# Kernel tuning notes

Hardware: AMD Instinct MI355X
Metric: run time of the kernel (lower is better)

The kernel has to match this reference:

```python
import jax, jax.numpy as jnp
import numpy as np
from jax import lax

B = 16
IMG = 384
P = 16
C = 3
DIM = 256
DEPTH = 6
HEADS = 4
DH = 64
INNER = HEADS * DH  # 256
MLP = 512
NC = 21
HP = IMG // P       # 24
N = HP * HP         # 576
PD = C * P * P      # 768
K = 16
SCALE = DH ** -0.5
NEG = -1e9


def _ln(x, g, b):
    mu = x.mean(-1, keepdims=True)
    var = ((x - mu) ** 2).mean(-1, keepdims=True)
    return (x - mu) / jnp.sqrt(var + 1e-5) * g + b


def _conv(x, w, b):
    y = lax.conv_general_dilated(x, w, (1, 1), 'SAME',
                                 dimension_numbers=('NCHW', 'OIHW', 'NCHW'))
    return y + b[None, :, None, None]


def _up2(x):
    b, c, h, w = x.shape
    return jax.image.resize(x, (b, c, 2 * h, 2 * w), 'bilinear')


def _attn(x, g, bt, qkv_w, out_w, out_b, alpha):
    xn = _ln(x, g, bt)
    qkv = xn @ qkv_w                              # [B,N,3*INNER]
    q, k, v = jnp.split(qkv, 3, axis=-1)
    def heads(t):
        return t.reshape(B, N, HEADS, DH).transpose(0, 2, 1, 3)  # b h n d
    q, k, v = heads(q), heads(k), heads(v)
    dots = jnp.einsum('bhid,bhjd->bhij', q, k) * SCALE           # [B,H,N,N]
    vals, idx = lax.top_k(dots, K)                               # [B,H,N,K]
    bi = jnp.arange(B)[:, None, None, None]
    hi = jnp.arange(HEADS)[None, :, None, None]
    ni = jnp.arange(N)[None, None, :, None]
    sparse = jnp.full(dots.shape, NEG, dots.dtype).at[bi, hi, ni, idx].set(vals)
    sparse_attn = jax.nn.softmax(sparse, axis=-1)
    global_attn = jax.nn.softmax(dots, axis=-1)
    a = jnp.clip(alpha, 0.0, 1.0)
    attn = (1 - a) * sparse_attn + a * global_attn
    out = jnp.einsum('bhij,bhjd->bhid', attn, v)                 # [B,H,N,DH]
    out = out.transpose(0, 2, 1, 3).reshape(B, N, INNER)
    return out @ out_w + out_b


def _forward(img, patch_w, patch_b, pos_emb,
             ln1_g, ln1_b, qkv_w, out_w, out_b, alpha,
             ln2_g, ln2_b, ff_w1, ff_b1, ff_w2, ff_b2,
             lnf_g, lnf_b,
             conv1_w, conv1_b, conv2_w, conv2_b, conv3_w, conv3_b):
    # patchify: b c (h p1) (w p2) -> b (h w) (p1 p2 c)
    x = img.reshape(B, C, HP, P, HP, P).transpose(0, 2, 4, 3, 5, 1).reshape(B, N, PD)
    x = x @ patch_w + patch_b + pos_emb
    for i in range(DEPTH):
        x = x + _attn(x, ln1_g[i], ln1_b[i], qkv_w[i], out_w[i], out_b[i], alpha[i])
        h = _ln(x, ln2_g[i], ln2_b[i])
        h = jax.nn.gelu(h @ ff_w1[i] + ff_b1[i], approximate=False)
        x = x + h @ ff_w2[i] + ff_b2[i]
    x = _ln(x, lnf_g, lnf_b)
    x = x.transpose(0, 2, 1).reshape(B, DIM, HP, HP)             # b d h w
    x = jax.nn.relu(_conv(x, conv1_w, conv1_b))
    x = _up2(x)
    x = jax.nn.relu(_conv(x, conv2_w, conv2_b))
    x = _up2(x)
    x = _conv(x, conv3_w, conv3_b)
    return jax.image.resize(x, (B, NC, IMG, IMG), 'bilinear')


def setup_inputs() -> dict:
    key = jax.random.key(0)
    ks = jax.random.split(key, 16)
    s = 0.02
    d = {
        'img': jax.random.normal(ks[0], (B, C, IMG, IMG), jnp.float32),
        'patch_w': jax.random.normal(ks[1], (PD, DIM)) * s,
        'patch_b': jnp.zeros((DIM,)),
        'pos_emb': jax.random.normal(ks[2], (1, N, DIM)) * s,
        'ln1_g': jnp.ones((DEPTH, DIM)), 'ln1_b': jnp.zeros((DEPTH, DIM)),
        'qkv_w': jax.random.normal(ks[3], (DEPTH, DIM, 3 * INNER)) * s,
        'out_w': jax.random.normal(ks[4], (DEPTH, INNER, DIM)) * s,
        'out_b': jnp.zeros((DEPTH, DIM)),
        'alpha': jnp.full((DEPTH,), 0.2),
        'ln2_g': jnp.ones((DEPTH, DIM)), 'ln2_b': jnp.zeros((DEPTH, DIM)),
        'ff_w1': jax.random.normal(ks[5], (DEPTH, DIM, MLP)) * s,
        'ff_b1': jnp.zeros((DEPTH, MLP)),
        'ff_w2': jax.random.normal(ks[6], (DEPTH, MLP, DIM)) * s,
        'ff_b2': jnp.zeros((DEPTH, DIM)),
        'lnf_g': jnp.ones((DIM,)), 'lnf_b': jnp.zeros((DIM,)),
        'conv1_w': jax.random.normal(ks[7], (DIM // 2, DIM, 3, 3)) * s,
        'conv1_b': jnp.zeros((DIM // 2,)),
        'conv2_w': jax.random.normal(ks[8], (DIM // 4, DIM // 2, 3, 3)) * s,
        'conv2_b': jnp.zeros((DIM // 4,)),
        'conv3_w': jax.random.normal(ks[9], (NC, DIM // 4, 1, 1)) * s,
        'conv3_b': jnp.zeros((NC,)),
    }
    return d


def reference(img, patch_w, patch_b, pos_emb,
              ln1_g, ln1_b, qkv_w, out_w, out_b, alpha,
              ln2_g, ln2_b, ff_w1, ff_b1, ff_w2, ff_b2,
              lnf_g, lnf_b,
              conv1_w, conv1_b, conv2_w, conv2_b, conv3_w, conv3_b):
    return _forward(img, patch_w, patch_b, pos_emb,
                    ln1_g, ln1_b, qkv_w, out_w, out_b, alpha,
                    ln2_g, ln2_b, ff_w1, ff_b1, ff_w2, ff_b2,
                    lnf_g, lnf_b,
                    conv1_w, conv1_b, conv2_w, conv2_b, conv3_w, conv3_b)
```

## Files before the change

kernel.cpp:

```cpp
#include <hip/hip_runtime.h>
#include <cfloat>
#include <cmath>

constexpr int NB    = 16;
constexpr int IMGSZ = 384;
constexpr int PSZ   = 16;
constexpr int NCH   = 3;
constexpr int DMODEL= 256;
constexpr int DEPTH = 6;
constexpr int NHEAD = 4;
constexpr int DHEAD = 64;
constexpr int DQKV  = 768;
constexpr int DMLP  = 512;
constexpr int NCLS  = 21;
constexpr int HPATCH= 24;
constexpr int NTOK  = 576;
constexpr int NPD   = 768;
constexpr int TOPK  = 16;
constexpr int NROWS = NB * NTOK;
constexpr int OUT_TOTAL = NB * NCLS * IMGSZ * IMGSZ;

constexpr int RPB    = 16;
constexpr int NBLK   = NTOK / RPB;
constexpr int CHUNK  = 64;
constexpr int NCHUNK = NTOK / CHUNK;
constexpr int SCP    = 577;

typedef __attribute__((ext_vector_type(8))) short bf16x8;
typedef __attribute__((ext_vector_type(4))) float f32x4;

__device__ __forceinline__ unsigned short f2bf(float f) {
    unsigned u = __builtin_bit_cast(unsigned, f);
    unsigned r = (u + 0x7FFFu + ((u >> 16) & 1u)) >> 16;
    return (unsigned short)r;
}
__device__ __forceinline__ float bf2f(unsigned short h) {
    unsigned u = ((unsigned)h) << 16;
    return __builtin_bit_cast(float, u);
}

__global__ __launch_bounds__(256) void k_castT(const float* __restrict__ src,
                                               unsigned short* __restrict__ dst,
                                               int K, int N) {
    int t = blockIdx.x * 256 + threadIdx.x;
    if (t >= K * N) return;
    size_t base = (size_t)blockIdx.y * K * N;
    int n = t / K, k = t - n * K;
    dst[base + t] = f2bf(src[base + (size_t)k * N + n]);
}

template <int IC>
__global__ __launch_bounds__(256) void k_castConv(const float* __restrict__ src,
                                                  unsigned short* __restrict__ dst,
                                                  int OC) {
    int t = blockIdx.x * 256 + threadIdx.x;
    if (t >= OC * 9 * IC) return;
    int oc = t / (9 * IC);
    int r = t - oc * 9 * IC;
    int tap = r / IC, ic = r - tap * IC;
    dst[t] = f2bf(src[((size_t)(oc * IC + ic)) * 9 + tap]);
}

__global__ __launch_bounds__(256) void k_patchify(const float* __restrict__ img,
                                                  unsigned short* __restrict__ A) {
    int t = blockIdx.x * 256 + threadIdx.x;
    if (t >= NROWS * NPD) return;
    int r  = t / NPD, pd = t - r * NPD;
    int b  = r / NTOK, n = r - b * NTOK;
    int hy = n / HPATCH, hx = n - hy * HPATCH;
    int c  = pd % NCH;  int q = pd / NCH;
    int p2 = q % PSZ;   int p1 = q / PSZ;
    A[t] = f2bf(img[(((size_t)(b * NCH + c)) * IMGSZ + hy * PSZ + p1) * IMGSZ + hx * PSZ + p2]);
}

template <int BM, int BN, int EPI, int CIN>
__global__ __launch_bounds__(256) void k_mm(
    const unsigned short* __restrict__ Abf,
    const unsigned short* __restrict__ Wt,
    const float* __restrict__ bias,
    const float* __restrict__ extra,
    float* __restrict__ outf,
    unsigned short* __restrict__ outb,
    unsigned short* __restrict__ outb2,
    int M, int Nn, int K, int H, int Wd, int gxd, int gyd)
{
    constexpr int MF = BM / 32;
    constexpr int NF = BN / 32;
    constexpr bool GATHER = (CIN > 0);
    constexpr int AREP = BM * 4 / 256;
    constexpr int BREP = BN * 4 / 256;
    __shared__ __align__(16) short As[4][BM][8];
    __shared__ __align__(16) short Bs[4][BN][8];
    const int tid = threadIdx.x;
    const int p = blockIdx.x;
    const int xr = p & 7, xq = p >> 3;
    const int bm = (xr * (gyd >> 3) + xq / gxd) * BM;
    const int bn = (xq % gxd) * BN;
    const int lane = tid & 63, wid = tid >> 6;
    const int wm = wid >> 1, wn = wid & 1;

    int pb_[AREP], py_[AREP], px_[AREP];
    if (GATHER) {
        #pragma unroll
        for (int rep = 0; rep < AREP; ++rep) {
            int idx = rep * 256 + tid;
            int m = idx >> 2;
            int pix = bm + m;
            px_[rep] = pix % Wd;
            int r = pix / Wd;
            py_[rep] = r % H;
            pb_[rep] = r / H;
        }
    }

    f32x4 acc[MF][NF];
    #pragma unroll
    for (int i = 0; i < MF; ++i)
        #pragma unroll
        for (int j = 0; j < NF; ++j)
            acc[i][j] = (f32x4){0.f, 0.f, 0.f, 0.f};

    for (int k0 = 0; k0 < K; k0 += 32) {
        #pragma unroll
        for (int rep = 0; rep < AREP; ++rep) {
            int idx = rep * 256 + tid;
            int m = idx >> 2, kg = idx & 3;
            if (!GATHER) {
                *(bf16x8*)As[kg][m] =
                    *(const bf16x8*)(Abf + (size_t)(bm + m) * K + k0 + kg * 8);
            } else {
                int k = k0 + kg * 8;
                int tap = k / CIN;
                int ic = k - tap * CIN;
                int dy = tap / 3 - 1, dx = tap % 3 - 1;
                int yy = py_[rep] + dy, xx = px_[rep] + dx;
                bf16x8 v = (bf16x8){0, 0, 0, 0, 0, 0, 0, 0};
                if ((unsigned)yy < (unsigned)H && (unsigned)xx < (unsigned)Wd)
                    v = *(const bf16x8*)(Abf +
                        ((size_t)((pb_[rep] * H + yy) * Wd + xx)) * CIN + ic);
                *(bf16x8*)As[kg][m] = v;
            }
        }
        #pragma unroll
        for (int rep = 0; rep < BREP; ++rep) {
            int idx = rep * 256 + tid;
            int n = idx >> 2, kg = idx & 3;
            *(bf16x8*)Bs[kg][n] =
                *(const bf16x8*)(Wt + (size_t)(bn + n) * K + k0 + kg * 8);
        }
        __syncthreads();
        bf16x8 af[MF], bfv[NF];
        #pragma unroll
        for (int i = 0; i < MF; ++i)
            af[i] = *(const bf16x8*)As[lane >> 4][wm * (BM / 2) + i * 16 + (lane & 15)];
        #pragma unroll
        for (int j = 0; j < NF; ++j)
            bfv[j] = *(const bf16x8*)Bs[lane >> 4][wn * (BN / 2) + j * 16 + (lane & 15)];
        #pragma unroll
        for (int i = 0; i < MF; ++i)
            #pragma unroll
            for (int j = 0; j < NF; ++j)
                acc[i][j] = __builtin_amdgcn_mfma_f32_16x16x32_bf16(
                    af[i], bfv[j], acc[i][j], 0, 0, 0);
        __syncthreads();
    }

    #pragma unroll
    for (int i = 0; i < MF; ++i) {
        const int row0 = bm + wm * (BM / 2) + i * 16 + (lane >> 4) * 4;
        #pragma unroll
        for (int j = 0; j < NF; ++j) {
            const int col = bn + wn * (BN / 2) + j * 16 + (lane & 15);
            #pragma unroll
            for (int r = 0; r < 4; ++r) {
                const int rr = row0 + r;
                float v = acc[i][j][r];
                if (EPI >= 1 && EPI <= 4) v += bias[col];
                if (EPI == 1) v += outf[(size_t)rr * Nn + col];
                if (EPI == 2) v = 0.5f * v * (1.0f + erff(v * 0.70710678118f));
                if (EPI == 3) v += extra[(size_t)(rr % NTOK) * Nn + col];
                if (EPI == 4) v = fmaxf(v, 0.f);
                if (EPI == 2 || EPI == 4) {
                    outb[(size_t)rr * Nn + col] = f2bf(v);
                } else if (EPI == 5) {
                    unsigned short hi = f2bf(v);
                    outb[(size_t)rr * Nn + col] = hi;
                    outb2[(size_t)rr * Nn + col] = f2bf(v - bf2f(hi));
                } else {
                    outf[(size_t)rr * Nn + col] = v;
                }
            }
        }
    }
}

__global__ __launch_bounds__(256) void k_ln(const float* __restrict__ x,
                                            const float* __restrict__ g,
                                            const float* __restrict__ bb,
                                            unsigned short* __restrict__ y) {
    const int row = blockIdx.x, tid = threadIdx.x;
    float v = x[(size_t)row * DMODEL + tid];
    float s = v;
    #pragma unroll
    for (int off = 32; off; off >>= 1) s += __shfl_xor(s, off);
    __shared__ float ls[4], ls2[4];
    if ((tid & 63) == 0) ls[tid >> 6] = s;
    __syncthreads();
    float mu = (ls[0] + ls[1] + ls[2] + ls[3]) * (1.0f / DMODEL);
    float d = v - mu;
    float qq = d * d;
    #pragma unroll
    for (int off = 32; off; off >>= 1) qq += __shfl_xor(qq, off);
    if ((tid & 63) == 0) ls2[tid >> 6] = qq;
    __syncthreads();
    float var = (ls2[0] + ls2[1] + ls2[2] + ls2[3]) * (1.0f / DMODEL);
    y[(size_t)row * DMODEL + tid] = f2bf(d * rsqrtf(var + 1e-5f) * g[tid] + bb[tid]);
}

__global__ __launch_bounds__(256) void k_vT(const unsigned short* __restrict__ qhi,
                                            const unsigned short* __restrict__ qlo,
                                            unsigned short* __restrict__ vthi,
                                            unsigned short* __restrict__ vtlo) {
    __shared__ short tile[2][64][66];
    const int c = blockIdx.x, h = blockIdx.y, b = blockIdx.z;
    const int tid = threadIdx.x;
    #pragma unroll
    for (int rep = 0; rep < 4; ++rep) {
        int idx = rep * 256 + tid;
        int hl = idx >> 9, rem = idx & 511, n = rem >> 3, dg = rem & 7;
        const unsigned short* src = (hl ? qlo : qhi) +
            (size_t)(b * NTOK + c * CHUNK + n) * DQKV + 2 * DMODEL + h * DHEAD + dg * 8;
        bf16x8 v = *(const bf16x8*)src;
        #pragma unroll
        for (int e = 0; e < 8; ++e) tile[hl][dg * 8 + e][n] = v[e];
    }
    __syncthreads();
    #pragma unroll
    for (int rep = 0; rep < 4; ++rep) {
        int idx = rep * 256 + tid;
        int hl = idx >> 9, rem = idx & 511, d = rem >> 3, np = rem & 7;
        bf16x8 o;
        #pragma unroll
        for (int e = 0; e < 8; ++e) o[e] = tile[hl][d][np * 8 + e];
        *(bf16x8*)((hl ? vtlo : vthi) +
                   (size_t)((b * NHEAD + h) * DHEAD + d) * NTOK + c * CHUNK + np * 8) = o;
    }
}

struct KF { bf16x8 h0, h1, l0, l1; };
__device__ __forceinline__ KF ldkf(const unsigned short* __restrict__ hi,
                                   const unsigned short* __restrict__ lo,
                                   size_t off) {
    KF f;
    f.h0 = *(const bf16x8*)(hi + off);
    f.h1 = *(const bf16x8*)(hi + off + 32);
    f.l0 = *(const bf16x8*)(lo + off);
    f.l1 = *(const bf16x8*)(lo + off + 32);
    return f;
}

__global__ __launch_bounds__(256, 4) void k_attn(
    const unsigned short* __restrict__ qhi,
    const unsigned short* __restrict__ qlo,
    const unsigned short* __restrict__ vthi,
    const unsigned short* __restrict__ vtlo,
    const float* __restrict__ alpha_l,
    unsigned short* __restrict__ ao) {
    __shared__ __align__(16) unsigned char ub[16 * SCP * 4];
    float* scp = (float*)ub;
    short* pj  = (short*)ub;

    const int tid = threadIdx.x;
    const int lane = tid & 63;
    const int ct = tid >> 6;
    const int l15 = lane & 15, lg = lane >> 4;
    const int xr = blockIdx.x & 7, xq = blockIdx.x >> 3;
    const int g = xr + 8 * (xq / NBLK);
    const int b = g >> 2, h = g & 3;
    const int i0 = (xq % NBLK) * RPB;

    bf16x8 aqh0, aqh1, aql0, aql1;
    {
        const size_t qoff = (size_t)(b * NTOK + i0 + l15) * DQKV + h * DHEAD + lg * 8;
        aqh0 = *(const bf16x8*)(qhi + qoff);
        aqh1 = *(const bf16x8*)(qhi + qoff + 32);
        aql0 = *(const bf16x8*)(qlo + qoff);
        aql1 = *(const bf16x8*)(qlo + qoff + 32);
    }

    const size_t kRow = (size_t)(b * NTOK + ct * 16 + l15) * DQKV + DMODEL + h * DHEAD + lg * 8;
    KF kc = ldkf(qhi, qlo, kRow);
    #pragma unroll
    for (int c = 0; c < NCHUNK; ++c) {
        KF kn;
        if (c + 1 < NCHUNK)
            kn = ldkf(qhi, qlo, kRow + (size_t)(c + 1) * CHUNK * DQKV);
        f32x4 sD = (f32x4){0.f, 0.f, 0.f, 0.f};
        sD = __builtin_amdgcn_mfma_f32_16x16x32_bf16(aqh0, kc.h0, sD, 0, 0, 0);
        sD = __builtin_amdgcn_mfma_f32_16x16x32_bf16(aqh0, kc.l0, sD, 0, 0, 0);
        sD = __builtin_amdgcn_mfma_f32_16x16x32_bf16(aql0, kc.h0, sD, 0, 0, 0);
        sD = __builtin_amdgcn_mfma_f32_16x16x32_bf16(aqh1, kc.h1, sD, 0, 0, 0);
        sD = __builtin_amdgcn_mfma_f32_16x16x32_bf16(aqh1, kc.l1, sD, 0, 0, 0);
        sD = __builtin_amdgcn_mfma_f32_16x16x32_bf16(aql1, kc.h1, sD, 0, 0, 0);
        const int col = c * CHUNK + ct * 16 + l15;
        #pragma unroll
        for (int r = 0; r < 4; ++r)
            scp[(lg * 4 + r) * SCP + col] = sD[r] * 0.125f;
        if (c + 1 < NCHUNK) kc = kn;
    }
    __syncthreads();

    float o_[4][9];
    const int wrow = ct * 4;
    #pragma unroll
    for (int rr = 0; rr < 4; ++rr)
        #pragma unroll
        for (int t = 0; t < 9; ++t)
            o_[rr][t] = scp[(wrow + rr) * SCP + t * 64 + lane];
    __syncthreads();

    unsigned msk[4] = {0u, 0u, 0u, 0u};
    float M_[4];
    for (int k = 0; k < TOPK; ++k) {
        float lm[4];
        #pragma unroll
        for (int rr = 0; rr < 4; ++rr) {
            float m0 = -FLT_MAX;
            #pragma unroll
            for (int t = 0; t < 9; ++t) {
                float v = ((msk[rr] >> t) & 1u) ? -FLT_MAX : o_[rr][t];
                m0 = fmaxf(m0, v);
            }
            lm[rr] = m0;
        }
        #pragma unroll
        for (int off = 1; off < 64; off <<= 1) {
            #pragma unroll
            for (int rr = 0; rr < 4; ++rr)
                lm[rr] = fmaxf(lm[rr], __shfl_xor(lm[rr], off));
        }
        if (k == 0) {
            #pragma unroll
            for (int rr = 0; rr < 4; ++rr) M_[rr] = lm[rr];
        }
        #pragma unroll
        for (int rr = 0; rr < 4; ++rr) {
            int js = -1;
            #pragma unroll
            for (int t = 0; t < 9; ++t) {
                if (js < 0) {
                    unsigned long long bal =
                        __ballot((((msk[rr] >> t) & 1u) == 0u) && (o_[rr][t] == lm[rr]));
                    if (bal) js = t * 64 + (int)__builtin_ctzll(bal);
                }
            }
            if ((js & 63) == lane) msk[rr] |= 1u << (js >> 6);
        }
    }

    const float al = fminf(fmaxf(alpha_l[0], 0.f), 1.f);
    float gs[4], ss[4];
    #pragma unroll
    for (int rr = 0; rr < 4; ++rr) {
        float g_ = 0.f, s_ = 0.f;
        #pragma unroll
        for (int t = 0; t < 9; ++t) {
            float e = __expf(o_[rr][t] - M_[rr]);
            g_ += e;
            if ((msk[rr] >> t) & 1u) s_ += e;
        }
        gs[rr] = g_; ss[rr] = s_;
    }
    #pragma unroll
    for (int off = 1; off < 64; off <<= 1) {
        #pragma unroll
        for (int rr = 0; rr < 4; ++rr) {
            gs[rr] += __shfl_xor(gs[rr], off);
            ss[rr] += __shfl_xor(ss[rr], off);
        }
    }
    float ca[4], cs[4];
    #pragma unroll
    for (int rr = 0; rr < 4; ++rr) {
        ca[rr] = al / gs[rr];
        cs[rr] = (1.f - al) / ss[rr];
    }

    const size_t vRow = (size_t)((b * NHEAD + h) * DHEAD + ct * 16 + l15) * NTOK + lg * 8;
    KF vc = ldkf(vthi, vtlo, vRow);
    f32x4 acc = (f32x4){0.f, 0.f, 0.f, 0.f};
    #pragma unroll
    for (int c = 0; c < NCHUNK; ++c) {
        KF vn;
        if (c + 1 < NCHUNK)
            vn = ldkf(vthi, vtlo, vRow + (size_t)(c + 1) * CHUNK);
        short* pb = pj + (c & 1) * (2 * 16 * 72);
        #pragma unroll
        for (int rr = 0; rr < 4; ++rr) {
            float e = __expf(o_[rr][c] - M_[rr]);
            float wv = e * (ca[rr] + (((msk[rr] >> c) & 1u) ? cs[rr] : 0.f));
            unsigned short hi = f2bf(wv);
            pb[(wrow + rr) * 72 + lane] = (short)hi;
            pb[16 * 72 + (wrow + rr) * 72 + lane] = (short)f2bf(wv - bf2f(hi));
        }
        __syncthreads();
        const short* pr = pb + l15 * 72 + lg * 8;
        bf16x8 ah0 = *(const bf16x8*)(pr);
        bf16x8 ah1 = *(const bf16x8*)(pr + 32);
        bf16x8 al0 = *(const bf16x8*)(pr + 16 * 72);
        bf16x8 al1 = *(const bf16x8*)(pr + 16 * 72 + 32);
        acc = __builtin_amdgcn_mfma_f32_16x16x32_bf16(ah0, vc.h0, acc, 0, 0, 0);
        acc = __builtin_amdgcn_mfma_f32_16x16x32_bf16(ah0, vc.l0, acc, 0, 0, 0);
        acc = __builtin_amdgcn_mfma_f32_16x16x32_bf16(al0, vc.h0, acc, 0, 0, 0);
        acc = __builtin_amdgcn_mfma_f32_16x16x32_bf16(ah1, vc.h1, acc, 0, 0, 0);
        acc = __builtin_amdgcn_mfma_f32_16x16x32_bf16(ah1, vc.l1, acc, 0, 0, 0);
        acc = __builtin_amdgcn_mfma_f32_16x16x32_bf16(al1, vc.h1, acc, 0, 0, 0);
        if (c + 1 < NCHUNK) vc = vn;
    }
    {
        const int qrow = i0 + lg * 4;
        const int dcol = h * DHEAD + ct * 16 + l15;
        #pragma unroll
        for (int r = 0; r < 4; ++r)
            ao[(size_t)(b * NTOK + qrow + r) * DMODEL + dcol] = f2bf(acc[r]);
    }
}

__device__ __forceinline__ void bilin_axis(float sF, int H, int& i0, int& i1, float& f) {
    float fl = floorf(sF);
    f = sF - fl;
    int lo = (int)fl;
    i0 = lo < 0 ? 0 : (lo > H - 1 ? H - 1 : lo);
    int hi = lo + 1;
    i1 = hi < 0 ? 0 : (hi > H - 1 ? H - 1 : hi);
}

__global__ __launch_bounds__(256) void k_up2n(const unsigned short* __restrict__ in,
                                              unsigned short* __restrict__ outp,
                                              int Hin, int C) {
    const int Ho = 2 * Hin;
    const int CG = C / 8;
    const int total = NB * Ho * Ho * CG;
    int t = blockIdx.x * 256 + threadIdx.x;
    if (t >= total) return;
    int cg = t % CG; int r = t / CG;
    int x = r % Ho; r /= Ho;
    int y = r % Ho; int b = r / Ho;
    int i0, i1, j0, j1; float fy, fx;
    bilin_axis(0.5f * y - 0.25f, Hin, i0, i1, fy);
    bilin_axis(0.5f * x - 0.25f, Hin, j0, j1, fx);
    const unsigned short* base = in + (size_t)b * Hin * Hin * C + cg * 8;
    const bf16x8 p00 = *(const bf16x8*)(base + (size_t)(i0 * Hin + j0) * C);
    const bf16x8 p01 = *(const bf16x8*)(base + (size_t)(i0 * Hin + j1) * C);
    const bf16x8 p10 = *(const bf16x8*)(base + (size_t)(i1 * Hin + j0) * C);
    const bf16x8 p11 = *(const bf16x8*)(base + (size_t)(i1 * Hin + j1) * C);
    bf16x8 o;
    #pragma unroll
    for (int e = 0; e < 8; ++e) {
        float v = (1.f - fy) * ((1.f - fx) * bf2f((unsigned short)p00[e]) + fx * bf2f((unsigned short)p01[e]))
                + fy        * ((1.f - fx) * bf2f((unsigned short)p10[e]) + fx * bf2f((unsigned short)p11[e]));
        o[e] = (short)f2bf(v);
    }
    *(bf16x8*)(outp + (size_t)t * 8) = o;
}

__global__ __launch_bounds__(256) void k_conv3n(const unsigned short* __restrict__ in,
                                                const float* __restrict__ w,
                                                const float* __restrict__ bias,
                                                float* __restrict__ outp) {
    __shared__ float ws_[NCLS * 64];
    for (int i = threadIdx.x; i < NCLS * 64; i += 256) ws_[i] = w[i];
    __syncthreads();
    int t = blockIdx.x * 256 + threadIdx.x;
    if (t >= NB * 9216) return;
    int pix = t % 9216, b = t / 9216;
    float xv[64];
    const unsigned short* p = in + (size_t)t * 64;
    #pragma unroll
    for (int c = 0; c < 8; ++c) {
        bf16x8 v = *(const bf16x8*)(p + c * 8);
        #pragma unroll
        for (int e = 0; e < 8; ++e) xv[c * 8 + e] = bf2f((unsigned short)v[e]);
    }
    float* op = outp + (size_t)b * NCLS * 9216 + pix;
    #pragma unroll
    for (int o = 0; o < NCLS; ++o) {
        float acc = bias[o];
        #pragma unroll
        for (int ic = 0; ic < 64; ++ic) acc += ws_[o * 64 + ic] * xv[ic];
        op[(size_t)o * 9216] = acc;
    }
}

__global__ __launch_bounds__(256) void k_resize4(const float* __restrict__ in,
                                                 float* __restrict__ outp) {
    int t = blockIdx.x * 256 + threadIdx.x;
    if (t >= OUT_TOTAL) return;
    int x = t % IMGSZ; int r = t / IMGSZ; int y = r % IMGSZ; int bc = r / IMGSZ;
    int i0, i1, j0, j1; float fy, fx;
    bilin_axis(0.25f * y - 0.375f, 96, i0, i1, fy);
    bilin_axis(0.25f * x - 0.375f, 96, j0, j1, fx);
    const float* p = in + (size_t)bc * 9216;
    outp[t] = (1.f - fy) * ((1.f - fx) * p[i0 * 96 + j0] + fx * p[i0 * 96 + j1])
            + fy        * ((1.f - fx) * p[i1 * 96 + j0] + fx * p[i1 * 96 + j1]);
}

extern "C" void kernel_launch(void* const* d_in, const int* in_sizes, int n_in,
                              void* d_out, int out_size, void* d_ws, size_t ws_size,
                              hipStream_t stream) {
    const float* img     = (const float*)d_in[0];
    const float* patch_w = (const float*)d_in[1];
    const float* patch_b = (const float*)d_in[2];
    const float* pos_emb = (const float*)d_in[3];
    const float* ln1_g   = (const float*)d_in[4];
    const float* ln1_b   = (const float*)d_in[5];
    const float* qkv_w   = (const float*)d_in[6];
    const float* out_w   = (const float*)d_in[7];
    const float* out_b   = (const float*)d_in[8];
    const float* alpha   = (const float*)d_in[9];
    const float* ln2_g   = (const float*)d_in[10];
    const float* ln2_b   = (const float*)d_in[11];
    const float* ff_w1   = (const float*)d_in[12];
    const float* ff_b1   = (const float*)d_in[13];
    const float* ff_w2   = (const float*)d_in[14];
    const float* ff_b2   = (const float*)d_in[15];
    const float* lnf_g   = (const float*)d_in[16];
    const float* lnf_b   = (const float*)d_in[17];
    const float* conv1_w = (const float*)d_in[18];
    const float* conv1_b = (const float*)d_in[19];
    const float* conv2_w = (const float*)d_in[20];
    const float* conv2_b = (const float*)d_in[21];
    const float* conv3_w = (const float*)d_in[22];
    const float* conv3_b = (const float*)d_in[23];

    float* x = (float*)d_ws;
    unsigned short* qkv_hi = (unsigned short*)(x + (size_t)NROWS * DMODEL);
    unsigned short* qkv_lo = qkv_hi + (size_t)NROWS * DQKV;
    unsigned short* xn_bf  = qkv_lo + (size_t)NROWS * DQKV;
    unsigned short* ao_bf  = xn_bf + (size_t)NROWS * DMODEL;
    unsigned short* h_bf   = ao_bf + (size_t)NROWS * DMODEL;
    unsigned short* pA     = h_bf + (size_t)NROWS * DMLP;
    unsigned short* wts    = pA + (size_t)NROWS * NPD;
    unsigned short* pwt  = wts;
    unsigned short* qwt  = pwt  + 768 * 256;
    unsigned short* owt  = qwt  + 6 * 768 * 256;
    unsigned short* f1wt = owt  + 6 * 256 * 256;
    unsigned short* f2wt = f1wt + 6 * 256 * 512;
    unsigned short* c1wt = f2wt + 6 * 512 * 256;
    unsigned short* c2wt = c1wt + 128 * 9 * 256;
    unsigned short* vthi = c2wt + 64 * 9 * 128;
    unsigned short* vtlo = vthi + (size_t)64 * 64 * NTOK;
    unsigned short* c1n = ao_bf;
    unsigned short* u1n = h_bf;
    unsigned short* c2n = xn_bf;
    unsigned short* u2n = qkv_hi;
    float* c3 = (float*)pA;

    k_castT<<<dim3(768, 1), 256, 0, stream>>>(patch_w, pwt, NPD, DMODEL);
    k_castT<<<dim3(768, 6), 256, 0, stream>>>(qkv_w, qwt, DMODEL, DQKV);
    k_castT<<<dim3(256, 6), 256, 0, stream>>>(out_w, owt, DMODEL, DMODEL);
    k_castT<<<dim3(512, 6), 256, 0, stream>>>(ff_w1, f1wt, DMODEL, DMLP);
    k_castT<<<dim3(512, 6), 256, 0, stream>>>(ff_w2, f2wt, DMLP, DMODEL);
    k_castConv<256><<<1152, 256, 0, stream>>>(conv1_w, c1wt, 128);
    k_castConv<128><<<288, 256, 0, stream>>>(conv2_w, c2wt, 64);

    k_patchify<<<(NROWS * NPD + 255) / 256, 256, 0, stream>>>(img, pA);
    k_mm<128, 64, 3, 0><<<4 * 72, 256, 0, stream>>>(
        pA, pwt, patch_b, pos_emb, x, nullptr, nullptr, NROWS, DMODEL, NPD, 0, 0, 4, 72);

    for (int l = 0; l < DEPTH; ++l) {
        k_ln<<<NROWS, 256, 0, stream>>>(x, ln1_g + l * DMODEL, ln1_b + l * DMODEL, xn_bf);
        k_mm<128, 128, 5, 0><<<6 * 72, 256, 0, stream>>>(
            xn_bf, qwt + (size_t)l * DQKV * DMODEL, nullptr, nullptr,
            nullptr, qkv_hi, qkv_lo, NROWS, DQKV, DMODEL, 0, 0, 6, 72);
        k_vT<<<dim3(NCHUNK, NHEAD, NB), 256, 0, stream>>>(qkv_hi, qkv_lo, vthi, vtlo);
        k_attn<<<NBLK * NHEAD * NB, 256, 0, stream>>>(
            qkv_hi, qkv_lo, vthi, vtlo, alpha + l, ao_bf);
        k_mm<128, 64, 1, 0><<<4 * 72, 256, 0, stream>>>(
            ao_bf, owt + (size_t)l * DMODEL * DMODEL, out_b + l * DMODEL, nullptr,
            x, nullptr, nullptr, NROWS, DMODEL, DMODEL, 0, 0, 4, 72);
        k_ln<<<NROWS, 256, 0, stream>>>(x, ln2_g + l * DMODEL, ln2_b + l * DMODEL, xn_bf);
        k_mm<128, 128, 2, 0><<<4 * 72, 256, 0, stream>>>(
            xn_bf, f1wt + (size_t)l * DMLP * DMODEL, ff_b1 + l * DMLP, nullptr,
            nullptr, h_bf, nullptr, NROWS, DMLP, DMODEL, 0, 0, 4, 72);
        k_mm<128, 64, 1, 0><<<4 * 72, 256, 0, stream>>>(
            h_bf, f2wt + (size_t)l * DMODEL * DMLP, ff_b2 + l * DMODEL, nullptr,
            x, nullptr, nullptr, NROWS, DMODEL, DMLP, 0, 0, 4, 72);
    }

    k_ln<<<NROWS, 256, 0, stream>>>(x, lnf_g, lnf_b, xn_bf);
    k_mm<64, 128, 4, 256><<<1 * 144, 256, 0, stream>>>(
        xn_bf, c1wt, conv1_b, nullptr, nullptr, c1n, nullptr, NROWS, 128, 9 * 256, 24, 24, 1, 144);
    k_up2n<<<(NB * 48 * 48 * 16 + 255) / 256, 256, 0, stream>>>(c1n, u1n, 24, 128);
    k_mm<128, 64, 4, 128><<<1 * 288, 256, 0, stream>>>(
        u1n, c2wt, conv2_b, nullptr, nullptr, c2n, nullptr, NB * 48 * 48, 64, 9 * 128, 48, 48, 1, 288);
    k_up2n<<<(NB * 96 * 96 * 8 + 255) / 256, 256, 0, stream>>>(c2n, u2n, 48, 64);
    k_conv3n<<<(NB * 9216 + 255) / 256, 256, 0, stream>>>(u2n, conv3_w, conv3_b, c3);
    k_resize4<<<(OUT_TOTAL + 255) / 256, 256, 0, stream>>>(c3, (float*)d_out);
}
```

Baseline: 1.500 ms.

## Fuse LayerNorm into residual GEMMs and write transposed V from QKV GEMM

Adds a full-row GEMM kernel (32 rows by 256 columns) that applies bias and residual or positional embedding, writes x, and computes the following LayerNorm in its epilogue, which removes the standalone k_ln launches. The QKV GEMM epilogue now writes Q/K hi/lo into a narrower 512-wide buffer and scatters V directly into the transposed per-head layout, which removes the k_vT kernel. This cuts launches and global round trips. In exchange the fused GEMM uses small 32-row tiles that reload the full weight tile per block, and the transposed V stores are narrow 8-byte scattered writes.

```diff
diff --git a/kernel.cpp b/kernel.cpp
--- a/kernel.cpp
+++ b/kernel.cpp
@@ -11,6 +11,7 @@
 constexpr int NHEAD = 4;
 constexpr int DHEAD = 64;
 constexpr int DQKV  = 768;
+constexpr int QKS   = 512;
 constexpr int DMLP  = 512;
 constexpr int NCLS  = 21;
 constexpr int HPATCH= 24;
@@ -78,10 +79,11 @@
     const unsigned short* __restrict__ Abf,
     const unsigned short* __restrict__ Wt,
     const float* __restrict__ bias,
-    const float* __restrict__ extra,
     float* __restrict__ outf,
     unsigned short* __restrict__ outb,
     unsigned short* __restrict__ outb2,
+    unsigned short* __restrict__ vth,
+    unsigned short* __restrict__ vtl,
     int M, int Nn, int K, int H, int Wd, int gxd, int gyd)
 {
     constexpr int MF = BM / 32;
@@ -98,6 +100,7 @@
     const int bn = (xq % gxd) * BN;
     const int lane = tid & 63, wid = tid >> 6;
     const int wm = wid >> 1, wn = wid & 1;
+    const int l15 = lane & 15, lg = lane >> 4;
 
     int pb_[AREP], py_[AREP], px_[AREP];
     if (GATHER) {
@@ -152,10 +155,10 @@
         bf16x8 af[MF], bfv[NF];
         #pragma unroll
         for (int i = 0; i < MF; ++i)
-            af[i] = *(const bf16x8*)As[lane >> 4][wm * (BM / 2) + i * 16 + (lane & 15)];
+            af[i] = *(const bf16x8*)As[lg][wm * (BM / 2) + i * 16 + l15];
         #pragma unroll
         for (int j = 0; j < NF; ++j)
-            bfv[j] = *(const bf16x8*)Bs[lane >> 4][wn * (BN / 2) + j * 16 + (lane & 15)];
+            bfv[j] = *(const bf16x8*)Bs[lg][wn * (BN / 2) + j * 16 + l15];
         #pragma unroll
         for (int i = 0; i < MF; ++i)
             #pragma unroll
@@ -165,85 +168,200 @@
         __syncthreads();
     }
 
-    #pragma unroll
-    for (int i = 0; i < MF; ++i) {
-        const int row0 = bm + wm * (BM / 2) + i * 16 + (lane >> 4) * 4;
-        #pragma unroll
-        for (int j = 0; j < NF; ++j) {
-            const int col = bn + wn * (BN / 2) + j * 16 + (lane & 15);
-            #pragma unroll
-            for (int r = 0; r < 4; ++r) {
-                const int rr = row0 + r;
-                float v = acc[i][j][r];
-                if (EPI >= 1 && EPI <= 4) v += bias[col];
-                if (EPI == 1) v += outf[(size_t)rr * Nn + col];
-                if (EPI == 2) v = 0.5f * v * (1.0f + erff(v * 0.70710678118f));
-                if (EPI == 3) v += extra[(size_t)(rr % NTOK) * Nn + col];
-                if (EPI == 4) v = fmaxf(v, 0.f);
-                if (EPI == 2 || EPI == 4) {
-                    outb[(size_t)rr * Nn + col] = f2bf(v);
-                } else if (EPI == 5) {
-                    unsigned short hi = f2bf(v);
-                    outb[(size_t)rr * Nn + col] = hi;
-                    outb2[(size_t)rr * Nn + col] = f2bf(v - bf2f(hi));
+    if constexpr (EPI == 8) {
+        #pragma unroll
+        for (int i = 0; i < MF; ++i) {
+            const int row0 = bm + wm * (BM / 2) + i * 16 + lg * 4;
+            #pragma unroll
+            for (int j = 0; j < NF; ++j) {
+                const int col = bn + wn * (BN / 2) + j * 16 + l15;
+                if (col < 512) {
+                    #pragma unroll
+                    for (int r = 0; r < 4; ++r) {
+                        float v = acc[i][j][r];
+                        unsigned short hi = f2bf(v);
+                        outb[(size_t)(row0 + r) * QKS + col] = hi;
+                        outb2[(size_t)(row0 + r) * QKS + col] = f2bf(v - bf2f(hi));
+                    }
                 } else {
-                    outf[(size_t)rr * Nn + col] = v;
+                    const int d = col - 512, hh = d >> 6, dd = d & 63;
+                    const int bb = row0 / NTOK, n = row0 % NTOK;
+                    unsigned long long ph = 0ull, pl = 0ull;
+                    #pragma unroll
+                    for (int r = 0; r < 4; ++r) {
+                        float v = acc[i][j][r];
+                        unsigned short hi = f2bf(v);
+                        unsigned short lo = f2bf(v - bf2f(hi));
+                        ph |= (unsigned long long)hi << (16 * r);
+                        pl |= (unsigned long long)lo << (16 * r);
+                    }
+                    const size_t off = (size_t)((bb * NHEAD + hh) * DHEAD + dd) * NTOK + n;
+                    *(unsigned long long*)(vth + off) = ph;
+                    *(unsigned long long*)(vtl + off) = pl;
                 }
             }
         }
-    }
-}
-
-__global__ __launch_bounds__(256) void k_ln(const float* __restrict__ x,
-                                            const float* __restrict__ g,
-                                            const float* __restrict__ bb,
-                                            unsigned short* __restrict__ y) {
-    const int row = blockIdx.x, tid = threadIdx.x;
-    float v = x[(size_t)row * DMODEL + tid];
-    float s = v;
-    #pragma unroll
-    for (int off = 32; off; off >>= 1) s += __shfl_xor(s, off);
-    __shared__ float ls[4], ls2[4];
-    if ((tid & 63) == 0) ls[tid >> 6] = s;
+    } else {
+        #pragma unroll
+        for (int i = 0; i < MF; ++i) {
+            const int row0 = bm + wm * (BM / 2) + i * 16 + lg * 4;
+            #pragma unroll
+            for (int j = 0; j < NF; ++j) {
+                const int col = bn + wn * (BN / 2) + j * 16 + l15;
+                #pragma unroll
+                for (int r = 0; r < 4; ++r) {
+                    const int rr = row0 + r;
+                    float v = acc[i][j][r] + bias[col];
+                    if (EPI == 2) v = 0.5f * v * (1.0f + erff(v * 0.70710678118f));
+                    if (EPI == 4) v = fmaxf(v, 0.f);
+                    outb[(size_t)rr * Nn + col] = f2bf(v);
+                }
+            }
+        }
+    }
+}
+
+template <int RES>
+__global__ __launch_bounds__(256) void k_gemm_ln(
+    const unsigned short* __restrict__ Abf,
+    const unsigned short* __restrict__ Wt,
+    const float* __restrict__ bias,
+    const float* __restrict__ extra,
+    const float* __restrict__ lng,
+    const float* __restrict__ lnb,
+    float* __restrict__ x,
+    unsigned short* __restrict__ xn,
+    int K, int gyd)
+{
+    constexpr int BM = 32;
+    __shared__ __align__(16) short As[4][BM][8];
+    __shared__ __align__(16) short Bs[4][256][8];
+    __shared__ float redS[BM][4];
+    __shared__ float redQ[BM][4];
+    const int tid = threadIdx.x;
+    const int p = blockIdx.x;
+    const int xr = p & 7, xq = p >> 3;
+    const int bm = (xr * (gyd >> 3) + xq) * BM;
+    const int lane = tid & 63, wn = tid >> 6;
+    const int l15 = lane & 15, lg = lane >> 4;
+
+    f32x4 acc[2][4];
+    #pragma unroll
+    for (int i = 0; i < 2; ++i)
+        #pragma unroll
+        for (int j = 0; j < 4; ++j)
+            acc[i][j] = (f32x4){0.f, 0.f, 0.f, 0.f};
+
+    for (int k0 = 0; k0 < K; k0 += 32) {
+        if (tid < BM * 4) {
+            int m = tid >> 2, kg = tid & 3;
+            *(bf16x8*)As[kg][m] = *(const bf16x8*)(Abf + (size_t)(bm + m) * K + k0 + kg * 8);
+        }
+        #pragma unroll
+        for (int rep = 0; rep < 4; ++rep) {
+            int idx = rep * 256 + tid;
+            int n = idx >> 2, kg = idx & 3;
+            *(bf16x8*)Bs[kg][n] = *(const bf16x8*)(Wt + (size_t)n * K + k0 + kg * 8);
+        }
+        __syncthreads();
+        bf16x8 af[2], bfv[4];
+        #pragma unroll
+        for (int i = 0; i < 2; ++i)
+            af[i] = *(const bf16x8*)As[lg][i * 16 + l15];
+        #pragma unroll
+        for (int j = 0; j < 4; ++j)
+            bfv[j] = *(const bf16x8*)Bs[lg][wn * 64 + j * 16 + l15];
+        #pragma unroll
+        for (int i = 0; i < 2; ++i)
+            #pragma unroll
+            for (int j = 0; j < 4; ++j)
+                acc[i][j] = __builtin_amdgcn_mfma_f32_16x16x32_bf16(
+                    af[i], bfv[j], acc[i][j], 0, 0, 0);
+        __syncthreads();
+    }
+
+    #pragma unroll
+    for (int i = 0; i < 2; ++i) {
+        #pragma unroll
+        for (int j = 0; j < 4; ++j) {
+            const int col = wn * 64 + j * 16 + l15;
+            #pragma unroll
+            for (int r = 0; r < 4; ++r) {
+                const int rr = bm + i * 16 + lg * 4 + r;
+                float v = acc[i][j][r] + bias[col];
+                if (RES) v += x[(size_t)rr * DMODEL + col];
+                else     v += extra[(size_t)(rr % NTOK) * DMODEL + col];
+                x[(size_t)rr * DMODEL + col] = v;
+                acc[i][j][r] = v;
+            }
+        }
+    }
+    float s[2][4];
+    #pragma unroll
+    for (int i = 0; i < 2; ++i)
+        #pragma unroll
+        for (int r = 0; r < 4; ++r)
+            s[i][r] = ((acc[i][0][r] + acc[i][1][r]) + acc[i][2][r]) + acc[i][3][r];
+    #pragma unroll
+    for (int off = 1; off < 16; off <<= 1)
+        #pragma unroll
+        for (int i = 0; i < 2; ++i)
+            #pragma unroll
+            for (int r = 0; r < 4; ++r)
+                s[i][r] += __shfl_xor(s[i][r], off);
+    if (l15 == 0)
+        #pragma unroll
+        for (int i = 0; i < 2; ++i)
+            #pragma unroll
+            for (int r = 0; r < 4; ++r)
+                redS[i * 16 + lg * 4 + r][wn] = s[i][r];
     __syncthreads();
-    float mu = (ls[0] + ls[1] + ls[2] + ls[3]) * (1.0f / DMODEL);
-    float d = v - mu;
-    float qq = d * d;
-    #pragma unroll
-    for (int off = 32; off; off >>= 1) qq += __shfl_xor(qq, off);
-    if ((tid & 63) == 0) ls2[tid >> 6] = qq;
+    float mu[2][4];
+    #pragma unroll
+    for (int i = 0; i < 2; ++i)
+        #pragma unroll
+        for (int r = 0; r < 4; ++r) {
+            const float* q = redS[i * 16 + lg * 4 + r];
+            mu[i][r] = (((q[0] + q[1]) + q[2]) + q[3]) * (1.0f / DMODEL);
+        }
+    float qq[2][4];
+    #pragma unroll
+    for (int i = 0; i < 2; ++i)
+        #pragma unroll
+        for (int r = 0; r < 4; ++r) {
+            float d0 = acc[i][0][r] - mu[i][r], d1 = acc[i][1][r] - mu[i][r];
+            float d2 = acc[i][2][r] - mu[i][r], d3 = acc[i][3][r] - mu[i][r];
+            qq[i][r] = ((d0 * d0 + d1 * d1) + d2 * d2) + d3 * d3;
+        }
+    #pragma unroll
+    for (int off = 1; off < 16; off <<= 1)
+        #pragma unroll
+        for (int i = 0; i < 2; ++i)
+            #pragma unroll
+            for (int r = 0; r < 4; ++r)
+                qq[i][r] += __shfl_xor(qq[i][r], off);
+    if (l15 == 0)
+        #pragma unroll
+        for (int i = 0; i < 2; ++i)
+            #pragma unroll
+            for (int r = 0; r < 4; ++r)
+                redQ[i * 16 + lg * 4 + r][wn] = qq[i][r];
     __syncthreads();
-    float var = (ls2[0] + ls2[1] + ls2[2] + ls2[3]) * (1.0f / DMODEL);
-    y[(size_t)row * DMODEL + tid] = f2bf(d * rsqrtf(var + 1e-5f) * g[tid] + bb[tid]);
-}
-
-__global__ __launch_bounds__(256) void k_vT(const unsigned short* __restrict__ qhi,
-                                            const unsigned short* __restrict__ qlo,
-                                            unsigned short* __restrict__ vthi,
-                                            unsigned short* __restrict__ vtlo) {
-    __shared__ short tile[2][64][66];
-    const int c = blockIdx.x, h = blockIdx.y, b = blockIdx.z;
-    const int tid = threadIdx.x;
-    #pragma unroll
-    for (int rep = 0; rep < 4; ++rep) {
-        int idx = rep * 256 + tid;
-        int hl = idx >> 9, rem = idx & 511, n = rem >> 3, dg = rem & 7;
-        const unsigned short* src = (hl ? qlo : qhi) +
-            (size_t)(b * NTOK + c * CHUNK + n) * DQKV + 2 * DMODEL + h * DHEAD + dg * 8;
-        bf16x8 v = *(const bf16x8*)src;
-        #pragma unroll
-        for (int e = 0; e < 8; ++e) tile[hl][dg * 8 + e][n] = v[e];
-    }
-    __syncthreads();
-    #pragma unroll
-    for (int rep = 0; rep < 4; ++rep) {
-        int idx = rep * 256 + tid;
-        int hl = idx >> 9, rem = idx & 511, d = rem >> 3, np = rem & 7;
-        bf16x8 o;
-        #pragma unroll
-        for (int e = 0; e < 8; ++e) o[e] = tile[hl][d][np * 8 + e];
-        *(bf16x8*)((hl ? vtlo : vthi) +
-                   (size_t)((b * NHEAD + h) * DHEAD + d) * NTOK + c * CHUNK + np * 8) = o;
+    #pragma unroll
+    for (int i = 0; i < 2; ++i) {
+        #pragma unroll
+        for (int r = 0; r < 4; ++r) {
+            const float* q = redQ[i * 16 + lg * 4 + r];
+            float var = (((q[0] + q[1]) + q[2]) + q[3]) * (1.0f / DMODEL);
+            float rstd = rsqrtf(var + 1e-5f);
+            const int rr = bm + i * 16 + lg * 4 + r;
+            #pragma unroll
+            for (int j = 0; j < 4; ++j) {
+                const int col = wn * 64 + j * 16 + l15;
+                float o = (acc[i][j][r] - mu[i][r]) * rstd * lng[col] + lnb[col];
+                xn[(size_t)rr * DMODEL + col] = f2bf(o);
+            }
+        }
     }
 }
 
@@ -281,20 +399,20 @@
 
     bf16x8 aqh0, aqh1, aql0, aql1;
     {
-        const size_t qoff = (size_t)(b * NTOK + i0 + l15) * DQKV + h * DHEAD + lg * 8;
+        const size_t qoff = (size_t)(b * NTOK + i0 + l15) * QKS + h * DHEAD + lg * 8;
         aqh0 = *(const bf16x8*)(qhi + qoff);
         aqh1 = *(const bf16x8*)(qhi + qoff + 32);
         aql0 = *(const bf16x8*)(qlo + qoff);
         aql1 = *(const bf16x8*)(qlo + qoff + 32);
     }
 
-    const size_t kRow = (size_t)(b * NTOK + ct * 16 + l15) * DQKV + DMODEL + h * DHEAD + lg * 8;
+    const size_t kRow = (size_t)(b * NTOK + ct * 16 + l15) * QKS + DMODEL + h * DHEAD + lg * 8;
     KF kc = ldkf(qhi, qlo, kRow);
     #pragma unroll
     for (int c = 0; c < NCHUNK; ++c) {
         KF kn;
         if (c + 1 < NCHUNK)
-            kn = ldkf(qhi, qlo, kRow + (size_t)(c + 1) * CHUNK * DQKV);
+            kn = ldkf(qhi, qlo, kRow + (size_t)(c + 1) * CHUNK * QKS);
         f32x4 sD = (f32x4){0.f, 0.f, 0.f, 0.f};
         sD = __builtin_amdgcn_mfma_f32_16x16x32_bf16(aqh0, kc.h0, sD, 0, 0, 0);
         sD = __builtin_amdgcn_mfma_f32_16x16x32_bf16(aqh0, kc.l0, sD, 0, 0, 0);
@@ -535,8 +653,8 @@
 
     float* x = (float*)d_ws;
     unsigned short* qkv_hi = (unsigned short*)(x + (size_t)NROWS * DMODEL);
-    unsigned short* qkv_lo = qkv_hi + (size_t)NROWS * DQKV;
-    unsigned short* xn_bf  = qkv_lo + (size_t)NROWS * DQKV;
+    unsigned short* qkv_lo = qkv_hi + (size_t)NROWS * QKS;
+    unsigned short* xn_bf  = qkv_lo + (size_t)NROWS * QKS;
     unsigned short* ao_bf  = xn_bf + (size_t)NROWS * DMODEL;
     unsigned short* h_bf   = ao_bf + (size_t)NROWS * DMODEL;
     unsigned short* pA     = h_bf + (size_t)NROWS * DMLP;
@@ -565,35 +683,37 @@
     k_castConv<128><<<288, 256, 0, stream>>>(conv2_w, c2wt, 64);
 
     k_patchify<<<(NROWS * NPD + 255) / 256, 256, 0, stream>>>(img, pA);
-    k_mm<128, 64, 3, 0><<<4 * 72, 256, 0, stream>>>(
-        pA, pwt, patch_b, pos_emb, x, nullptr, nullptr, NROWS, DMODEL, NPD, 0, 0, 4, 72);
+    k_gemm_ln<0><<<288, 256, 0, stream>>>(
+        pA, pwt, patch_b, pos_emb, ln1_g, ln1_b, x, xn_bf, NPD, 288);
 
     for (int l = 0; l < DEPTH; ++l) {
-        k_ln<<<NROWS, 256, 0, stream>>>(x, ln1_g + l * DMODEL, ln1_b + l * DMODEL, xn_bf);
-        k_mm<128, 128, 5, 0><<<6 * 72, 256, 0, stream>>>(
-            xn_bf, qwt + (size_t)l * DQKV * DMODEL, nullptr, nullptr,
-            nullptr, qkv_hi, qkv_lo, NROWS, DQKV, DMODEL, 0, 0, 6, 72);
-        k_vT<<<dim3(NCHUNK, NHEAD, NB), 256, 0, stream>>>(qkv_hi, qkv_lo, vthi, vtlo);
+        k_mm<128, 128, 8, 0><<<6 * 72, 256, 0, stream>>>(
+            xn_bf, qwt + (size_t)l * DQKV * DMODEL, nullptr,
+            nullptr, qkv_hi, qkv_lo, vthi, vtlo,
+            NROWS, DQKV, DMODEL, 0, 0, 6, 72);
         k_attn<<<NBLK * NHEAD * NB, 256, 0, stream>>>(
             qkv_hi, qkv_lo, vthi, vtlo, alpha + l, ao_bf);
-        k_mm<128, 64, 1, 0><<<4 * 72, 256, 0, stream>>>(
+        k_gemm_ln<1><<<288, 256, 0, stream>>>(
             ao_bf, owt + (size_t)l * DMODEL * DMODEL, out_b + l * DMODEL, nullptr,
-            x, nullptr, nullptr, NROWS, DMODEL, DMODEL, 0, 0, 4, 72);
-        k_ln<<<NROWS, 256, 0, stream>>>(x, ln2_g + l * DMODEL, ln2_b + l * DMODEL, xn_bf);
+            ln2_g + l * DMODEL, ln2_b + l * DMODEL, x, xn_bf, DMODEL, 288);
         k_mm<128, 128, 2, 0><<<4 * 72, 256, 0, stream>>>(
-            xn_bf, f1wt + (size_t)l * DMLP * DMODEL, ff_b1 + l * DMLP, nullptr,
-            nullptr, h_bf, nullptr, NROWS, DMLP, DMODEL, 0, 0, 4, 72);
-        k_mm<128, 64, 1, 0><<<4 * 72, 256, 0, stream>>>(
+            xn_bf, f1wt + (size_t)l * DMLP * DMODEL, ff_b1 + l * DMLP,
+            nullptr, h_bf, nullptr, nullptr, nullptr,
+            NROWS, DMLP, DMODEL, 0, 0, 4, 72);
+        const float* ng = (l + 1 < DEPTH) ? (ln1_g + (l + 1) * DMODEL) : lnf_g;
+        const float* nb = (l + 1 < DEPTH) ? (ln1_b + (l + 1) * DMODEL) : lnf_b;
+        k_gemm_ln<1><<<288, 256, 0, stream>>>(
             h_bf, f2wt + (size_t)l * DMODEL * DMLP, ff_b2 + l * DMODEL, nullptr,
-            x, nullptr, nullptr, NROWS, DMODEL, DMLP, 0, 0, 4, 72);
-    }
-
-    k_ln<<<NROWS, 256, 0, stream>>>(x, lnf_g, lnf_b, xn_bf);
+            ng, nb, x, xn_bf, DMLP, 288);
+    }
+
     k_mm<64, 128, 4, 256><<<1 * 144, 256, 0, stream>>>(
-        xn_bf, c1wt, conv1_b, nullptr, nullptr, c1n, nullptr, NROWS, 128, 9 * 256, 24, 24, 1, 144);
+        xn_bf, c1wt, conv1_b, nullptr, c1n, nullptr, nullptr, nullptr,
+        NROWS, 128, 9 * 256, 24, 24, 1, 144);
     k_up2n<<<(NB * 48 * 48 * 16 + 255) / 256, 256, 0, stream>>>(c1n, u1n, 24, 128);
     k_mm<128, 64, 4, 128><<<1 * 288, 256, 0, stream>>>(
-        u1n, c2wt, conv2_b, nullptr, nullptr, c2n, nullptr, NB * 48 * 48, 64, 9 * 128, 48, 48, 1, 288);
+        u1n, c2wt, conv2_b, nullptr, c2n, nullptr, nullptr, nullptr,
+        NB * 48 * 48, 64, 9 * 128, 48, 48, 1, 288);
     k_up2n<<<(NB * 96 * 96 * 8 + 255) / 256, 256, 0, stream>>>(c2n, u2n, 48, 64);
     k_conv3n<<<(NB * 9216 + 255) / 256, 256, 0, stream>>>(u2n, conv3_w, conv3_b, c3);
     k_resize4<<<(OUT_TOTAL + 255) / 256, 256, 0, stream>>>(c3, (float*)d_out);
```

After: 1.368 ms. 8.8% less time.
